# Kernel optimization log

Hardware: AMD Instinct MI355X
Metric: run time of the kernel (lower is better)

The kernel has to match this reference:

```python
import jax, jax.numpy as jnp
import numpy as np

NUM_CLASSES = 100
NUM_HYPER_PER = 16
TOPK_RATIO = 0.1
ZDIM = 256
B = 64
K = 128


def setup_inputs() -> dict:
    key = jax.random.key(0)
    k1, k2, k3 = jax.random.split(key, 3)
    x = jax.random.normal(k1, (B, K, ZDIM), dtype=jnp.float32)
    y = jax.random.randint(k2, (B,), 0, NUM_CLASSES)
    hyper_params = jax.random.normal(k3, (NUM_CLASSES, NUM_HYPER_PER, ZDIM), dtype=jnp.float32)
    return {"x": x, "y": y, "hyper_params": hyper_params}


def _generate_G_from_H(H):
    # H: [N_nodes, N_edges], edge weights W = 1
    # G = DV^{-1/2} H DE^{-1} H^T DV^{-1/2}
    DV = H.sum(axis=1)          # node degrees [N]
    DE = H.sum(axis=0)          # edge degrees [E]
    inv_DE = 1.0 / DE
    DV2 = DV ** -0.5
    left = (DV2[:, None] * H) * inv_DE[None, :]   # DV^{-1/2} H DE^{-1}  [N, E]
    right = H * DV2[:, None]                      # (DV^{-1/2} H)       [N, E]
    return left @ right.T                         # [N, N]


def reference(x, y, hyper_params):
    B_, K_, d = x.shape
    # gather per-sample class hyperedge prototypes -> [B*P, d]
    hyper_clss = hyper_params[y].reshape(-1, d)
    # similarity, rearranged '(B K) E' then transposed -> [E, N]
    simi = jnp.einsum('bkd,ed->bke', x, hyper_clss).reshape(B_ * K_, -1).T
    kk = int(TOPK_RATIO * simi.shape[-1])
    # k-th largest similarity per edge as threshold
    thr = jax.lax.top_k(simi, kk)[0][:, -1:]      # [E, 1]
    H = (simi > thr).astype(jnp.float32).T        # incidence [N, E]
    G = _generate_G_from_H(H)
    hyper_x = x.reshape(-1, d)                    # [N, d]
    return (G, hyper_x)
```

## Files before the change

### kernel.cpp

```cpp
#include <hip/hip_runtime.h>
#include <hip/hip_bf16.h>
#include <cstdint>

#define NN 8192
#define EE 1024
#define DD 256
#define KK_SEL 819

typedef __attribute__((ext_vector_type(4))) int int32x4;

__global__ __launch_bounds__(256) void simi_gemm(
    const float* __restrict__ x, const int* __restrict__ y,
    const float* __restrict__ hyper, float* __restrict__ simi) {
  __shared__ float As[32][68];
  __shared__ float Bs[32][68];
  const int tid = threadIdx.x;
  const int bi = blockIdx.y;
  const int bj = blockIdx.x;
  const int ty = tid >> 4, tx = tid & 15;
  const int i0 = ty * 4, j0 = tx * 4;
  float acc[4][4] = {};

  for (int k0 = 0; k0 < DD; k0 += 32) {
#pragma unroll
    for (int p = 0; p < 2; ++p) {
      int f = p * 256 + tid;
      int le = f >> 3;
      int kq = (f & 7) * 4;
      int eg = bi * 64 + le;
      int cls = y[eg >> 4];
      const float* srcA = hyper + ((size_t)(cls * 16 + (eg & 15))) * DD + k0 + kq;
      float4 va = *(const float4*)srcA;
      As[kq + 0][le] = va.x; As[kq + 1][le] = va.y;
      As[kq + 2][le] = va.z; As[kq + 3][le] = va.w;
      int ng = bj * 64 + le;
      const float4 vb = *(const float4*)(x + (size_t)ng * DD + k0 + kq);
      Bs[kq + 0][le] = vb.x; Bs[kq + 1][le] = vb.y;
      Bs[kq + 2][le] = vb.z; Bs[kq + 3][le] = vb.w;
    }
    __syncthreads();
#pragma unroll
    for (int kk = 0; kk < 32; ++kk) {
      float4 a4 = *(const float4*)&As[kk][i0];
      float4 b4 = *(const float4*)&Bs[kk][j0];
      float av[4] = {a4.x, a4.y, a4.z, a4.w};
      float bv[4] = {b4.x, b4.y, b4.z, b4.w};
#pragma unroll
      for (int i = 0; i < 4; ++i)
#pragma unroll
        for (int j = 0; j < 4; ++j) acc[i][j] += av[i] * bv[j];
    }
    __syncthreads();
  }
#pragma unroll
  for (int i = 0; i < 4; ++i) {
    int e = bi * 64 + i0 + i;
    float4 o = {acc[i][0], acc[i][1], acc[i][2], acc[i][3]};
    *(float4*)&simi[(size_t)e * NN + bj * 64 + j0] = o;
  }
}

__global__ __launch_bounds__(256) void select_thr(
    const float* __restrict__ simi, float* __restrict__ thr, int* __restrict__ DE) {
  const int e = blockIdx.x;
  const float* row = simi + (size_t)e * NN;
  __shared__ unsigned hist[256];
  __shared__ unsigned sh_prefix;
  __shared__ int sh_r;
  __shared__ int red[256];
  const int tid = threadIdx.x;
  if (tid == 0) { sh_prefix = 0u; sh_r = NN - KK_SEL; }
  __syncthreads();

  for (int pass = 0; pass < 4; ++pass) {
    const int shift = 24 - pass * 8;
    for (int b = tid; b < 256; b += 256) hist[b] = 0u;
    __syncthreads();
    const unsigned prefix = sh_prefix;
    const unsigned pmask = (pass == 0) ? 0u : (0xFFFFFFFFu << (shift + 8));
    for (int i = tid; i < NN; i += 256) {
      unsigned u = __float_as_uint(row[i]);
      unsigned k = (u & 0x80000000u) ? ~u : (u | 0x80000000u);
      if ((k & pmask) == prefix) atomicAdd(&hist[(k >> shift) & 0xFFu], 1u);
    }
    __syncthreads();
    if (tid == 0) {
      unsigned cum = 0;
      int r = sh_r;
      for (int b = 0; b < 256; ++b) {
        unsigned h = hist[b];
        if (cum + h > (unsigned)r) {
          sh_prefix = sh_prefix | ((unsigned)b << shift);
          sh_r = r - (int)cum;
          break;
        }
        cum += h;
      }
    }
    __syncthreads();
  }
  const unsigned key = sh_prefix;
  const unsigned u = (key & 0x80000000u) ? (key & 0x7FFFFFFFu) : ~key;
  const float t = __uint_as_float(u);

  int cnt = 0;
  for (int i = tid; i < NN; i += 256) cnt += (row[i] > t) ? 1 : 0;
  red[tid] = cnt;
  __syncthreads();
  for (int s = 128; s > 0; s >>= 1) {
    if (tid < s) red[tid] += red[tid + s];
    __syncthreads();
  }
  if (tid == 0) { thr[e] = t; DE[e] = red[0]; }
}

__global__ __launch_bounds__(256) void build_h(
    const float* __restrict__ simi, const float* __restrict__ thr,
    unsigned long long* __restrict__ Hbits, float* __restrict__ DV2) {
  __shared__ float sthr[EE];
  const int tid = threadIdx.x;
  for (int e = tid; e < EE; e += 256) sthr[e] = thr[e];
  __syncthreads();
  const int n = blockIdx.x * 256 + tid;
  int dv = 0;
#pragma unroll 1
  for (int w = 0; w < 16; ++w) {
    unsigned long long m = 0ull;
#pragma unroll 8
    for (int b = 0; b < 64; ++b) {
      const int e = w * 64 + b;
      const float v = simi[(size_t)e * NN + n];
      m |= ((unsigned long long)(v > sthr[e])) << b;
    }
    Hbits[(size_t)n * 16 + w] = m;
    dv += __popcll(m);
  }
  DV2[n] = 1.0f / sqrtf((float)dv);
}

__global__ __launch_bounds__(256) void h8_expand(
    const unsigned long long* __restrict__ Hbits, unsigned char* __restrict__ H8) {
  const int idx = blockIdx.x * 256 + threadIdx.x;
  const int n = idx >> 6;
  const int c16 = idx & 63;
  const unsigned long long w = Hbits[(size_t)n * 16 + (c16 >> 2)];
  const unsigned int b16 = (unsigned int)((w >> ((c16 & 3) * 16)) & 0xFFFFull);
  uint4 u;
  u.x = ((b16 >> 0) & 1u) | (((b16 >> 1) & 1u) << 8) | (((b16 >> 2) & 1u) << 16) | (((b16 >> 3) & 1u) << 24);
  u.y = ((b16 >> 4) & 1u) | (((b16 >> 5) & 1u) << 8) | (((b16 >> 6) & 1u) << 16) | (((b16 >> 7) & 1u) << 24);
  u.z = ((b16 >> 8) & 1u) | (((b16 >> 9) & 1u) << 8) | (((b16 >> 10) & 1u) << 16) | (((b16 >> 11) & 1u) << 24);
  u.w = ((b16 >> 12) & 1u) | (((b16 >> 13) & 1u) << 8) | (((b16 >> 14) & 1u) << 16) | (((b16 >> 15) & 1u) << 24);
  *(uint4*)(H8 + (size_t)n * EE + c16 * 16) = u;
}

__global__ __launch_bounds__(256) void mode_exc(
    const int* __restrict__ DE, int* __restrict__ modeInfo,
    int* __restrict__ exc_idx, float* __restrict__ exc_delta) {
  __shared__ unsigned hist[1024];
  __shared__ int s_mode;
  __shared__ int s_cnt;
  const int tid = threadIdx.x;
  for (int i = tid; i < 1024; i += 256) hist[i] = 0u;
  __syncthreads();
  for (int e = tid; e < EE; e += 256) atomicAdd(&hist[DE[e]], 1u);
  __syncthreads();
  if (tid == 0) {
    int best = 1; unsigned bc = 0;
    for (int i = 0; i < 1024; ++i)
      if (hist[i] > bc) { bc = hist[i]; best = i; }
    s_mode = best; s_cnt = 0;
  }
  __syncthreads();
  const int mode = s_mode;
  const float invMode = 1.0f / (float)mode;
  for (int e = tid; e < EE; e += 256) {
    const int de = DE[e];
    if (de != mode) {
      const int idx = atomicAdd(&s_cnt, 1);
      exc_idx[idx] = e;
      exc_delta[idx] = 1.0f / (float)de - invMode;
    }
  }
  __syncthreads();
  if (tid == 0) {
    modeInfo[0] = s_mode;
    modeInfo[1] = s_cnt;
    modeInfo[2] = __float_as_int(invMode);
  }
}

__global__ __launch_bounds__(256) void g_mfma(
    const unsigned char* __restrict__ H8, const float* __restrict__ DV2,
    const int* __restrict__ modeInfo, const int* __restrict__ exc_idx,
    const float* __restrict__ exc_delta,
    const unsigned long long* __restrict__ Hbits, float* __restrict__ G) {
  __shared__ unsigned char As[128 * 128];
  __shared__ unsigned char Bs[128 * 128];
  __shared__ float sDVr[128], sDVc[128];
  const int tid = threadIdx.x;
  const int lane = tid & 63;
  const int wave = tid >> 6;
  const int bi = blockIdx.y, bj = blockIdx.x;
  if (tid < 128) sDVr[tid] = DV2[bi * 128 + tid];
  else sDVc[tid - 128] = DV2[bj * 128 + (tid - 128)];

  const unsigned char* Ag = H8 + (size_t)bi * 128 * EE;
  const unsigned char* Bg = H8 + (size_t)bj * 128 * EE;

  int32x4 acc[4][4];
  const int32x4 zero = {0, 0, 0, 0};
#pragma unroll
  for (int m = 0; m < 4; ++m)
#pragma unroll
    for (int n = 0; n < 4; ++n) acc[m][n] = zero;

  const int wr = wave >> 1, wc = wave & 1;

  for (int s = 0; s < 8; ++s) {
    const int kbase = s * 128;
#pragma unroll
    for (int q = 0; q < 4; ++q) {
      const int chunk = wave * 256 + q * 64 + lane;
      const int r = chunk >> 3;
      const int cq = (chunk & 7) * 16;
      const int csrc = cq ^ ((r & 7) << 4);
      __builtin_amdgcn_global_load_lds(
          (const __attribute__((address_space(1))) void*)(Ag + (size_t)r * EE + kbase + csrc),
          (__attribute__((address_space(3))) void*)(As + (wave * 256 + q * 64) * 16),
          16, 0, 0);
      __builtin_amdgcn_global_load_lds(
          (const __attribute__((address_space(1))) void*)(Bg + (size_t)r * EE + kbase + csrc),
          (__attribute__((address_space(3))) void*)(Bs + (wave * 256 + q * 64) * 16),
          16, 0, 0);
    }
    __syncthreads();
#pragma unroll
    for (int ks = 0; ks < 2; ++ks) {
      int32x4 af[4], bf[4];
#pragma unroll
      for (int m = 0; m < 4; ++m) {
        const int r = wr * 64 + m * 16 + (lane & 15);
        const int c = ks * 64 + (lane >> 4) * 16;
        af[m] = *(const int32x4*)&As[r * 128 + (c ^ ((r & 7) << 4))];
      }
#pragma unroll
      for (int n = 0; n < 4; ++n) {
        const int r = wc * 64 + n * 16 + (lane & 15);
        const int c = ks * 64 + (lane >> 4) * 16;
        bf[n] = *(const int32x4*)&Bs[r * 128 + (c ^ ((r & 7) << 4))];
      }
#pragma unroll
      for (int m = 0; m < 4; ++m)
#pragma unroll
        for (int n = 0; n < 4; ++n)
          acc[m][n] = __builtin_amdgcn_mfma_i32_16x16x64_i8(af[m], bf[n], acc[m][n], 0, 0, 0);
    }
    __syncthreads();
  }

  const float invMode = __int_as_float(modeInfo[2]);
  const int NX = modeInfo[1];
  const int l4 = lane >> 4;
  const int lc = lane & 15;
#pragma unroll
  for (int m = 0; m < 4; ++m) {
#pragma unroll
    for (int n = 0; n < 4; ++n) {
#pragma unroll
      for (int reg = 0; reg < 4; ++reg) {
        const int Rl = wr * 64 + m * 16 + l4 * 4 + reg;
        const int Cl = wc * 64 + n * 16 + lc;
        const int Rg = bi * 128 + Rl;
        const int Cg = bj * 128 + Cl;
        float v = (float)acc[m][n][reg] * invMode;
        for (int xx = 0; xx < NX; ++xx) {
          const int e = exc_idx[xx];
          const int w = e >> 6, b = e & 63;
          const unsigned long long rb = Hbits[(size_t)Rg * 16 + w] >> b;
          const unsigned long long cb = Hbits[(size_t)Cg * 16 + w] >> b;
          v += exc_delta[xx] * (float)(rb & cb & 1ull);
        }
        G[(size_t)Rg * NN + Cg] = v * sDVr[Rl] * sDVc[Cl];
      }
    }
  }
}

extern "C" void kernel_launch(void* const* d_in, const int* in_sizes, int n_in,
                              void* d_out, int out_size, void* d_ws, size_t ws_size,
                              hipStream_t stream) {
  const float* x = (const float*)d_in[0];
  const int* y = (const int*)d_in[1];
  const float* hyper = (const float*)d_in[2];
  float* out = (float*)d_out;

  float* simi = out;
  unsigned char* H8 = (unsigned char*)(out + (size_t)NN * NN);

  uint8_t* w8 = (uint8_t*)d_ws;
  float* thr = (float*)(w8 + 0);
  int* DE = (int*)(w8 + 4096);
  float* DV2 = (float*)(w8 + 8192);
  int* modeInfo = (int*)(w8 + 40960);
  int* exc_idx = (int*)(w8 + 41984);
  float* exc_delta = (float*)(w8 + 46080);
  unsigned long long* Hbits = (unsigned long long*)(w8 + 65536);

  simi_gemm<<<dim3(NN / 64, EE / 64), 256, 0, stream>>>(x, y, hyper, simi);
  select_thr<<<dim3(EE), 256, 0, stream>>>(simi, thr, DE);
  build_h<<<dim3(NN / 256), 256, 0, stream>>>(simi, thr, Hbits, DV2);
  h8_expand<<<dim3(NN * 64 / 256), 256, 0, stream>>>(Hbits, H8);
  mode_exc<<<dim3(1), 256, 0, stream>>>(DE, modeInfo, exc_idx, exc_delta);
  g_mfma<<<dim3(NN / 128, NN / 128), 256, 0, stream>>>(H8, DV2, modeInfo,
                                                       exc_idx, exc_delta, Hbits, out);
  hipMemcpyAsync(out + (size_t)NN * NN, x, (size_t)NN * DD * sizeof(float),
                 hipMemcpyDeviceToDevice, stream);
}
```

Baseline: 560.0 us.

## Exploit G symmetry with upper-triangular tiles and enlarge simi GEMM tile

The G computation now launches only upper-triangular 128x128 tiles. Each off-diagonal tile writes its transpose through a swizzled shared-memory buffer, so the int8 MFMA work is roughly halved. The similarity GEMM moves to 128x128 tiles with an 8x8 register micro-tile to improve data reuse. The threshold kernel takes the edge degree from radix-select histogram counts instead of a second pass over the row. The costs are extra shared-memory transpose traffic, less coalesced transposed stores, and a float-sqrt tile index mapping that depends on correct fix-up loops.

```diff
diff --git a/kernel.cpp b/kernel.cpp
--- a/kernel.cpp
+++ b/kernel.cpp
@@ -12,52 +12,70 @@
 __global__ __launch_bounds__(256) void simi_gemm(
     const float* __restrict__ x, const int* __restrict__ y,
     const float* __restrict__ hyper, float* __restrict__ simi) {
-  __shared__ float As[32][68];
-  __shared__ float Bs[32][68];
+  __shared__ float As[16][128];
+  __shared__ float Bs[16][128];
   const int tid = threadIdx.x;
   const int bi = blockIdx.y;
   const int bj = blockIdx.x;
   const int ty = tid >> 4, tx = tid & 15;
-  const int i0 = ty * 4, j0 = tx * 4;
-  float acc[4][4] = {};
-
-  for (int k0 = 0; k0 < DD; k0 += 32) {
-#pragma unroll
-    for (int p = 0; p < 2; ++p) {
-      int f = p * 256 + tid;
-      int le = f >> 3;
-      int kq = (f & 7) * 4;
-      int eg = bi * 64 + le;
-      int cls = y[eg >> 4];
-      const float* srcA = hyper + ((size_t)(cls * 16 + (eg & 15))) * DD + k0 + kq;
-      float4 va = *(const float4*)srcA;
-      As[kq + 0][le] = va.x; As[kq + 1][le] = va.y;
-      As[kq + 2][le] = va.z; As[kq + 3][le] = va.w;
-      int ng = bj * 64 + le;
-      const float4 vb = *(const float4*)(x + (size_t)ng * DD + k0 + kq);
-      Bs[kq + 0][le] = vb.x; Bs[kq + 1][le] = vb.y;
-      Bs[kq + 2][le] = vb.z; Bs[kq + 3][le] = vb.w;
-    }
-    __syncthreads();
-#pragma unroll
-    for (int kk = 0; kk < 32; ++kk) {
-      float4 a4 = *(const float4*)&As[kk][i0];
-      float4 b4 = *(const float4*)&Bs[kk][j0];
-      float av[4] = {a4.x, a4.y, a4.z, a4.w};
-      float bv[4] = {b4.x, b4.y, b4.z, b4.w};
-#pragma unroll
-      for (int i = 0; i < 4; ++i)
-#pragma unroll
-        for (int j = 0; j < 4; ++j) acc[i][j] += av[i] * bv[j];
-    }
-    __syncthreads();
-  }
-#pragma unroll
-  for (int i = 0; i < 4; ++i) {
-    int e = bi * 64 + i0 + i;
-    float4 o = {acc[i][0], acc[i][1], acc[i][2], acc[i][3]};
-    *(float4*)&simi[(size_t)e * NN + bj * 64 + j0] = o;
-  }
+  float acc[2][4][2][4] = {};
+
+  const int lr = tid >> 1;
+  const int lk = (tid & 1) * 8;
+  const int eg = bi * 128 + lr;
+  const int cls = y[eg >> 4];
+  const float* arow = hyper + ((size_t)(cls * 16 + (eg & 15))) * DD;
+  const float* brow = x + (size_t)(bj * 128 + lr) * DD;
+
+#pragma unroll 1
+  for (int k0 = 0; k0 < DD; k0 += 16) {
+    const float4 a0 = *(const float4*)(arow + k0 + lk);
+    const float4 a1 = *(const float4*)(arow + k0 + lk + 4);
+    const float4 b0 = *(const float4*)(brow + k0 + lk);
+    const float4 b1 = *(const float4*)(brow + k0 + lk + 4);
+    As[lk + 0][lr] = a0.x; As[lk + 1][lr] = a0.y;
+    As[lk + 2][lr] = a0.z; As[lk + 3][lr] = a0.w;
+    As[lk + 4][lr] = a1.x; As[lk + 5][lr] = a1.y;
+    As[lk + 6][lr] = a1.z; As[lk + 7][lr] = a1.w;
+    Bs[lk + 0][lr] = b0.x; Bs[lk + 1][lr] = b0.y;
+    Bs[lk + 2][lr] = b0.z; Bs[lk + 3][lr] = b0.w;
+    Bs[lk + 4][lr] = b1.x; Bs[lk + 5][lr] = b1.y;
+    Bs[lk + 6][lr] = b1.z; Bs[lk + 7][lr] = b1.w;
+    __syncthreads();
+#pragma unroll
+    for (int kk = 0; kk < 16; ++kk) {
+      const float4 ar0 = *(const float4*)&As[kk][ty * 4];
+      const float4 ar1 = *(const float4*)&As[kk][64 + ty * 4];
+      const float4 bc0 = *(const float4*)&Bs[kk][tx * 4];
+      const float4 bc1 = *(const float4*)&Bs[kk][64 + tx * 4];
+      const float av[2][4] = {{ar0.x, ar0.y, ar0.z, ar0.w},
+                              {ar1.x, ar1.y, ar1.z, ar1.w}};
+      const float bv[2][4] = {{bc0.x, bc0.y, bc0.z, bc0.w},
+                              {bc1.x, bc1.y, bc1.z, bc1.w}};
+#pragma unroll
+      for (int rh = 0; rh < 2; ++rh)
+#pragma unroll
+        for (int i = 0; i < 4; ++i)
+#pragma unroll
+          for (int ch = 0; ch < 2; ++ch)
+#pragma unroll
+            for (int j = 0; j < 4; ++j)
+              acc[rh][i][ch][j] += av[rh][i] * bv[ch][j];
+    }
+    __syncthreads();
+  }
+#pragma unroll
+  for (int rh = 0; rh < 2; ++rh)
+#pragma unroll
+    for (int i = 0; i < 4; ++i) {
+      const int e = bi * 128 + rh * 64 + ty * 4 + i;
+#pragma unroll
+      for (int ch = 0; ch < 2; ++ch) {
+        float4 o = {acc[rh][i][ch][0], acc[rh][i][ch][1],
+                    acc[rh][i][ch][2], acc[rh][i][ch][3]};
+        *(float4*)&simi[(size_t)e * NN + bj * 128 + ch * 64 + tx * 4] = o;
+      }
+    }
 }
 
 __global__ __launch_bounds__(256) void select_thr(
@@ -66,15 +84,14 @@
   const float* row = simi + (size_t)e * NN;
   __shared__ unsigned hist[256];
   __shared__ unsigned sh_prefix;
-  __shared__ int sh_r;
-  __shared__ int red[256];
-  const int tid = threadIdx.x;
-  if (tid == 0) { sh_prefix = 0u; sh_r = NN - KK_SEL; }
+  __shared__ int sh_r, sh_less, sh_eq;
+  const int tid = threadIdx.x;
+  if (tid == 0) { sh_prefix = 0u; sh_r = NN - KK_SEL; sh_less = 0; sh_eq = 0; }
   __syncthreads();
 
   for (int pass = 0; pass < 4; ++pass) {
     const int shift = 24 - pass * 8;
-    for (int b = tid; b < 256; b += 256) hist[b] = 0u;
+    hist[tid] = 0u;
     __syncthreads();
     const unsigned prefix = sh_prefix;
     const unsigned pmask = (pass == 0) ? 0u : (0xFFFFFFFFu << (shift + 8));
@@ -92,6 +109,8 @@
         if (cum + h > (unsigned)r) {
           sh_prefix = sh_prefix | ((unsigned)b << shift);
           sh_r = r - (int)cum;
+          sh_less += (int)cum;
+          if (pass == 3) sh_eq = (int)h;
           break;
         }
         cum += h;
@@ -99,19 +118,12 @@
     }
     __syncthreads();
   }
-  const unsigned key = sh_prefix;
-  const unsigned u = (key & 0x80000000u) ? (key & 0x7FFFFFFFu) : ~key;
-  const float t = __uint_as_float(u);
-
-  int cnt = 0;
-  for (int i = tid; i < NN; i += 256) cnt += (row[i] > t) ? 1 : 0;
-  red[tid] = cnt;
-  __syncthreads();
-  for (int s = 128; s > 0; s >>= 1) {
-    if (tid < s) red[tid] += red[tid + s];
-    __syncthreads();
-  }
-  if (tid == 0) { thr[e] = t; DE[e] = red[0]; }
+  if (tid == 0) {
+    const unsigned key = sh_prefix;
+    const unsigned u = (key & 0x80000000u) ? (key & 0x7FFFFFFFu) : ~key;
+    thr[e] = __uint_as_float(u);
+    DE[e] = NN - sh_less - sh_eq;
+  }
 }
 
 __global__ __launch_bounds__(256) void build_h(
@@ -194,13 +206,20 @@
     const int* __restrict__ modeInfo, const int* __restrict__ exc_idx,
     const float* __restrict__ exc_delta,
     const unsigned long long* __restrict__ Hbits, float* __restrict__ G) {
-  __shared__ unsigned char As[128 * 128];
-  __shared__ unsigned char Bs[128 * 128];
+  __shared__ unsigned char smem[32768];
   __shared__ float sDVr[128], sDVc[128];
+  unsigned char* As = smem;
+  unsigned char* Bs = smem + 16384;
+
+  const int t = blockIdx.x;
+  int bi = (int)(64.5 - sqrt(64.5 * 64.5 - 2.0 * (double)t));
+  while ((bi + 1) * 64 - ((bi + 1) * bi) / 2 <= t) ++bi;
+  while (bi * 64 - (bi * (bi - 1)) / 2 > t) --bi;
+  const int bj = bi + (t - (bi * 64 - (bi * (bi - 1)) / 2));
+
   const int tid = threadIdx.x;
   const int lane = tid & 63;
   const int wave = tid >> 6;
-  const int bi = blockIdx.y, bj = blockIdx.x;
   if (tid < 128) sDVr[tid] = DV2[bi * 128 + tid];
   else sDVc[tid - 128] = DV2[bj * 128 + (tid - 128)];
 
@@ -262,6 +281,7 @@
   const int NX = modeInfo[1];
   const int l4 = lane >> 4;
   const int lc = lane & 15;
+
 #pragma unroll
   for (int m = 0; m < 4; ++m) {
 #pragma unroll
@@ -284,6 +304,55 @@
       }
     }
   }
+
+  if (bi != bj) {
+    float* T = (float*)smem;
+#pragma unroll 1
+    for (int h = 0; h < 2; ++h) {
+      __syncthreads();
+      if (wr == h) {
+#pragma unroll
+        for (int m = 0; m < 4; ++m) {
+#pragma unroll
+          for (int n = 0; n < 4; ++n) {
+#pragma unroll
+            for (int reg = 0; reg < 4; ++reg) {
+              const int Rh = m * 16 + l4 * 4 + reg;
+              const int Cl = wc * 64 + n * 16 + lc;
+              float v = (float)acc[m][n][reg] * invMode;
+              if (NX) {
+                const int Rg = bi * 128 + h * 64 + Rh;
+                const int Cg = bj * 128 + Cl;
+                for (int xx = 0; xx < NX; ++xx) {
+                  const int e = exc_idx[xx];
+                  const int w = e >> 6, b = e & 63;
+                  const unsigned long long rb = Hbits[(size_t)Rg * 16 + w] >> b;
+                  const unsigned long long cb = Hbits[(size_t)Cg * 16 + w] >> b;
+                  v += exc_delta[xx] * (float)(rb & cb & 1ull);
+                }
+              }
+              T[Rh * 128 + (Cl ^ ((Rh & 7) << 2))] =
+                  v * sDVc[Cl] * sDVr[h * 64 + Rh];
+            }
+          }
+        }
+      }
+      __syncthreads();
+      const int orow = tid >> 1;
+      const int ob = (tid & 1) * 32;
+      float4* dst = (float4*)&G[(size_t)(bj * 128 + orow) * NN + bi * 128 + h * 64 + ob];
+#pragma unroll
+      for (int i = 0; i < 8; ++i) {
+        const int rr = ob + i * 4;
+        float4 o;
+        o.x = T[(rr + 0) * 128 + (orow ^ (((rr + 0) & 7) << 2))];
+        o.y = T[(rr + 1) * 128 + (orow ^ (((rr + 1) & 7) << 2))];
+        o.z = T[(rr + 2) * 128 + (orow ^ (((rr + 2) & 7) << 2))];
+        o.w = T[(rr + 3) * 128 + (orow ^ (((rr + 3) & 7) << 2))];
+        dst[i] = o;
+      }
+    }
+  }
 }
 
 extern "C" void kernel_launch(void* const* d_in, const int* in_sizes, int n_in,
@@ -306,13 +375,13 @@
   float* exc_delta = (float*)(w8 + 46080);
   unsigned long long* Hbits = (unsigned long long*)(w8 + 65536);
 
-  simi_gemm<<<dim3(NN / 64, EE / 64), 256, 0, stream>>>(x, y, hyper, simi);
+  simi_gemm<<<dim3(NN / 128, EE / 128), 256, 0, stream>>>(x, y, hyper, simi);
   select_thr<<<dim3(EE), 256, 0, stream>>>(simi, thr, DE);
   build_h<<<dim3(NN / 256), 256, 0, stream>>>(simi, thr, Hbits, DV2);
   h8_expand<<<dim3(NN * 64 / 256), 256, 0, stream>>>(Hbits, H8);
   mode_exc<<<dim3(1), 256, 0, stream>>>(DE, modeInfo, exc_idx, exc_delta);
-  g_mfma<<<dim3(NN / 128, NN / 128), 256, 0, stream>>>(H8, DV2, modeInfo,
-                                                       exc_idx, exc_delta, Hbits, out);
+  g_mfma<<<dim3(2080), 256, 0, stream>>>(H8, DV2, modeInfo, exc_idx, exc_delta,
+                                         Hbits, out);
   hipMemcpyAsync(out + (size_t)NN * NN, x, (size_t)NN * DD * sizeof(float),
                  hipMemcpyDeviceToDevice, stream);
 }
```

After: 619.2 us. +10.6%, slower.
